# Optimization experiments

Hardware: AMD Instinct MI355X
Metric: run time of the kernel (lower is better)

Reference implementation:

```python
import jax, jax.numpy as jnp
import numpy as np

ALPHA = 1.0
BETA = 2.0
GAMMA = 1.5  # PositionEffectFunction default (config.gamma is NOT passed through)
TEMPERATURE = 1.0


def position_matrix(L: int) -> jnp.ndarray:
    idx = jnp.arange(L, dtype=jnp.float32)
    dist = jnp.abs(idx[:, None] - idx[None, :]) / L  # normalized |i-j|/L
    base = jnp.exp(-BETA * dist)
    return ALPHA * (1.0 + GAMMA * base) / (1.0 + GAMMA)  # [L, L]


def setup_inputs() -> dict:
    key = jax.random.key(0)
    ks = jax.random.split(key, 10)
    B, S, D = 8, 2048, 1024
    std = 0.02
    return {
        "x": jax.random.normal(ks[0], (B, S, D), jnp.float32),
        "pos_emb": jax.random.normal(ks[1], (1, S, D), jnp.float32),
        "Wq": jax.random.normal(ks[2], (D, D), jnp.float32) * std,
        "bq": jax.random.normal(ks[3], (D,), jnp.float32) * std,
        "Wk": jax.random.normal(ks[4], (D, D), jnp.float32) * std,
        "bk": jax.random.normal(ks[5], (D,), jnp.float32) * std,
        "Wv": jax.random.normal(ks[6], (D, D), jnp.float32) * std,
        "bv": jax.random.normal(ks[7], (D,), jnp.float32) * std,
        "Wo": jax.random.normal(ks[8], (D, D), jnp.float32) * std,
        "bo": jax.random.normal(ks[9], (D,), jnp.float32) * std,
    }


def reference(x, pos_emb, Wq, bq, Wk, bk, Wv, bv, Wo, bo):
    B, S, D = x.shape
    x = x + pos_emb[:, :S, :]
    Q = x @ Wq + bq  # [B,S,D]
    K = x @ Wk + bk
    V = x @ Wv + bv
    scores = jnp.einsum("bsd,btd->bst", Q, K) / jnp.sqrt(jnp.float32(D))
    pw = position_matrix(S)  # [S,S], broadcast over batch
    scores = scores * pw[None, :, :] / TEMPERATURE
    attn = jax.nn.softmax(scores, axis=-1)  # [B,S,S]
    out = jnp.einsum("bst,btd->bsd", attn, V)
    out = out @ Wo + bo
    return out, attn
```

## Files before the change

kernel.cpp:

```cpp
#include <hip/hip_runtime.h>
#include <hip/hip_bf16.h>
#include <cstdint>

typedef _Float16 f16x8 __attribute__((ext_vector_type(8)));
typedef _Float16 f16x4 __attribute__((ext_vector_type(4)));
typedef float    f32x4 __attribute__((ext_vector_type(4)));

static constexpr int B = 8, S = 2048, D = 1024;
static constexpr long BSD = (long)B * S * D;
static constexpr long SD  = (long)S * D;
static constexpr long SS  = (long)S * S;
static constexpr long DD  = (long)D * D;

__device__ __forceinline__ void gload16(const void* g, void* l) {
  __builtin_amdgcn_global_load_lds(
      (const __attribute__((address_space(1))) void*)g,
      (__attribute__((address_space(3))) void*)l, 16, 0, 0);
}

#define CFENCE() asm volatile("" ::: "memory")

__global__ __launch_bounds__(256) void prep_x_kernel(
    const float* __restrict__ x, const float* __restrict__ pos,
    _Float16* __restrict__ xh) {
  long i = ((long)blockIdx.x * 256 + threadIdx.x) * 4;
  float4 xv = *(const float4*)(x + i);
  long p = i & (SD - 1);
  float4 pv = *(const float4*)(pos + p);
  f16x4 h;
  h.x = (_Float16)(xv.x + pv.x);
  h.y = (_Float16)(xv.y + pv.y);
  h.z = (_Float16)(xv.z + pv.z);
  h.w = (_Float16)(xv.w + pv.w);
  *(f16x4*)(xh + i) = h;
}

__global__ __launch_bounds__(256) void prep_w_kernel(
    const float* __restrict__ Wq, const float* __restrict__ Wk,
    const float* __restrict__ Wv, const float* __restrict__ Wo,
    _Float16* __restrict__ wqkv, _Float16* __restrict__ woh) {
  __shared__ _Float16 t[64][65];
  const int c0 = blockIdx.x * 64;
  const int r0 = blockIdx.y * 64;
  const int tid = threadIdx.x;
  const int lc = tid & 63;
  const int lr4 = tid >> 6;
  const float* srcs[4] = {Wq, Wk, Wv, Wo};
  #pragma unroll
  for (int m = 0; m < 4; ++m) {
    const float* src = srcs[m];
    _Float16* dst = (m < 3) ? (wqkv + (long)m * DD) : woh;
    #pragma unroll
    for (int ii = 0; ii < 16; ++ii) {
      int row = ii * 4 + lr4;
      t[lc][row] = (_Float16)src[(long)(r0 + row) * D + c0 + lc];
    }
    __syncthreads();
    #pragma unroll
    for (int ii = 0; ii < 16; ++ii) {
      int orow = ii * 4 + lr4;
      dst[(long)(c0 + orow) * D + r0 + lc] = t[orow][lc];
    }
    __syncthreads();
  }
}

__global__ __launch_bounds__(256) void prep_misc_kernel(
    const float* __restrict__ bq, const float* __restrict__ bk,
    const float* __restrict__ bv,
    float* __restrict__ bcat, float* __restrict__ pwtab) {
  int i = blockIdx.x * 256 + threadIdx.x;
  if (i < 3072) {
    float v = (i < 1024) ? bq[i] : (i < 2048) ? bk[i - 1024] : bv[i - 2048];
    bcat[i] = v;
  }
  int d = i - 3072;
  if (d >= 0 && d < 2048) {
    float dist = (float)d * (1.0f / 2048.0f);
    pwtab[d] = (1.0f + 1.5f * expf(-2.0f * dist)) * (1.0f / 2.5f) * (1.0f / 32.0f);
  }
}


enum { EPI_QKV = 0, EPI_SF16 = 1, EPI_PVO = 2, EPI_F32B = 3 };

__device__ __forceinline__ void stage_half(
    char* smem, const _Float16* mb, int off, int k64K, int sthb,
    int dst0, int dst1) {
  gload16(mb + off, smem + sthb + dst0);
  gload16(mb + off + k64K, smem + sthb + dst1);
}

__device__ __forceinline__ void rdA(const char* p, f16x8 (&af)[4][2]) {
#pragma unroll
  for (int mr = 0; mr < 4; ++mr)
#pragma unroll
    for (int kk = 0; kk < 2; ++kk)
      af[mr][kk] = *(const f16x8*)(p + mr * 2048 + kk * 1024);
}

__device__ __forceinline__ void rdB(const char* p, f16x8 (&bf)[2][2]) {
#pragma unroll
  for (int nr = 0; nr < 2; ++nr)
#pragma unroll
    for (int kk = 0; kk < 2; ++kk)
      bf[nr][kk] = *(const f16x8*)(p + nr * 2048 + kk * 1024);
}

__device__ __forceinline__ void mfma16(const f16x8 (&af)[4][2],
                                       const f16x8 (&bf)[2][2],
                                       f32x4 (&a4)[4][2]) {
#pragma unroll
  for (int kk = 0; kk < 2; ++kk)
#pragma unroll
    for (int mr = 0; mr < 4; ++mr)
#pragma unroll
      for (int nr = 0; nr < 2; ++nr)
        a4[mr][nr] = __builtin_amdgcn_mfma_f32_16x16x32_f16(
            af[mr][kk], bf[nr][kk], a4[mr][nr], 0, 0, 0);
}

template<int EPI>
__global__ __launch_bounds__(512, 2) void gemm256_kernel(
    const _Float16* __restrict__ A, const _Float16* __restrict__ Bt,
    const float* __restrict__ bias, const float* __restrict__ pwtab,
    float* __restrict__ outF,
    _Float16* __restrict__ o0, _Float16* __restrict__ o1, _Float16* __restrict__ o2,
    int M, int N, int K, long sA, long sB, long sC)
{
  __shared__ __align__(16) char smem[131072];
  const int tid = threadIdx.x;
  const int z = blockIdx.z;

  int bx = blockIdx.x, by = blockIdx.y;
  if (gridDim.z == 1) {
    const int bid = by * gridDim.x + bx;
    const int idx = bid >> 3;
    by = ((bid & 7) << 3) + (idx & 7);
    bx = idx >> 3;
  }
  const int rb = by * 256;
  const int cb = bx * 256;
  const _Float16* Ag = A + (long)z * sA + (long)rb * K;
  const _Float16* Bg = Bt + (long)z * sB + (long)cb * K;

  const int lane = tid & 63;
  const int wid = tid >> 6;
  const int lrin = lane & 15;
  const int lhi = lane >> 4;
  const int rtail = (lrin * 64 + lhi * 16) ^ (((lane >> 3) & 1) << 5);
  const int aoff = ((wid >> 2) * 4) * 2048 + rtail;
  const int boff = ((wid & 3) * 2) * 2048 + rtail;

  const int rin = lane >> 2;
  const int cinp = (lane & 3) ^ (((lane >> 5) & 1) << 1);
  const int rowc = (wid >> 1) * 16 + rin;
  const int colc = (wid & 1) * 32 + cinp * 8;
  const int stBase = rowc * K + colc;
  const int k64K = 64 * K;
  const int h128K = 128 * K;
  const int dst0 = tid * 16;
  const int dst1 = 8192 + tid * 16;

  const int NT = K >> 6;
  f32x4 acc00[4][2] = {}, acc01[4][2] = {}, acc11[4][2] = {}, acc10[4][2] = {};

  stage_half(smem, Ag, stBase,              k64K, 0,             dst0, dst1);
  stage_half(smem, Bg, stBase,              k64K, 32768,         dst0, dst1);
  stage_half(smem, Ag, stBase + h128K,      k64K, 16384,         dst0, dst1);
  stage_half(smem, Bg, stBase + h128K,      k64K, 49152,         dst0, dst1);
  stage_half(smem, Ag, stBase + 64,         k64K, 65536,         dst0, dst1);
  stage_half(smem, Bg, stBase + h128K + 64, k64K, 65536 + 49152, dst0, dst1);
  asm volatile("s_waitcnt vmcnt(4)" ::: "memory");
  __builtin_amdgcn_s_barrier();
  CFENCE();

  for (int t = 0; t < NT; ++t) {
    const int curbase = (t & 1) << 16;
    const int nxtbase = curbase ^ 65536;
    const bool s1ok = (t + 1) < NT;
    const bool s2ok = (t + 2) < NT;
    const int st1 = stBase + (t + 1) * 64;
    const int st2 = stBase + (t + 2) * 64;
    f16x8 af[4][2], bfA[2][2], bfB[2][2];

    rdA((const char*)smem + curbase + aoff, af);
    rdB((const char*)smem + curbase + 32768 + boff, bfA);
    if (s1ok) stage_half(smem, Ag, st1 + h128K, k64K, nxtbase + 16384, dst0, dst1);
    CFENCE();
    __builtin_amdgcn_s_barrier();
    CFENCE();
    __builtin_amdgcn_s_setprio(1);
    mfma16(af, bfA, acc00);
    __builtin_amdgcn_s_setprio(0);
    CFENCE();
    __builtin_amdgcn_s_barrier();
    CFENCE();

    rdB((const char*)smem + curbase + 49152 + boff, bfB);
    if (s1ok) stage_half(smem, Bg, st1, k64K, nxtbase + 32768, dst0, dst1);
    CFENCE();
    __builtin_amdgcn_s_barrier();
    CFENCE();
    __builtin_amdgcn_s_setprio(1);
    mfma16(af, bfB, acc01);
    __builtin_amdgcn_s_setprio(0);
    CFENCE();
    __builtin_amdgcn_s_barrier();
    CFENCE();

    rdA((const char*)smem + curbase + 16384 + aoff, af);
    if (s2ok) stage_half(smem, Ag, st2, k64K, curbase + 0, dst0, dst1);
    CFENCE();
    __builtin_amdgcn_s_barrier();
    CFENCE();
    __builtin_amdgcn_s_setprio(1);
    mfma16(af, bfB, acc11);
    __builtin_amdgcn_s_setprio(0);
    CFENCE();
    __builtin_amdgcn_s_barrier();
    CFENCE();

    rdB((const char*)smem + curbase + 32768 + boff, bfA);
    if (s2ok) stage_half(smem, Bg, st2 + h128K, k64K, curbase + 49152, dst0, dst1);
    CFENCE();
    __builtin_amdgcn_s_barrier();
    CFENCE();
    __builtin_amdgcn_s_setprio(1);
    mfma16(af, bfA, acc10);
    __builtin_amdgcn_s_setprio(0);
    if (s2ok) {
      asm volatile("s_waitcnt vmcnt(4)" ::: "memory");
    } else {
      asm volatile("s_waitcnt vmcnt(0)" ::: "memory");
    }
    __builtin_amdgcn_s_barrier();
    CFENCE();
  }

  const int wrow = (wid >> 2) * 64;
  const int wcol = (wid & 3) * 32;
  auto epi = [&](const f32x4 (&a4)[4][2], int qm, int qn) {
#pragma unroll
    for (int nr = 0; nr < 2; ++nr) {
      const int col = cb + qn * 128 + wcol + nr * 16 + lrin;
      float bv = 0.0f;
      if (EPI == EPI_QKV || EPI == EPI_F32B) bv = bias[col];
#pragma unroll
      for (int mr = 0; mr < 4; ++mr) {
        const int rowb = rb + qm * 128 + wrow + mr * 16 + lhi * 4;
        const f32x4 v4 = a4[mr][nr];
#pragma unroll
        for (int r = 0; r < 4; ++r) {
          const int row = rowb + r;
          const float v = v4[r];
          if (EPI == EPI_QKV) {
            const int matid = cb >> 10;
            _Float16* dst = (matid == 0) ? o0 : (matid == 1) ? o1 : o2;
            const int cl = col & 1023;
            const float vb = v + bv;
            if (matid < 2) {
              dst[(long)row * 1024 + cl] = (_Float16)vb;
            } else {
              const int bb = row >> 11;
              const int trow = row & (S - 1);
              dst[(long)bb * SD + (long)cl * S + trow] = (_Float16)vb;
            }
          } else if (EPI == EPI_SF16) {
            int dd = row - col; if (dd < 0) dd = -dd;
            o0[(long)z * sC + (long)row * N + col] = (_Float16)(v * pwtab[dd]);
          } else if (EPI == EPI_PVO) {
            o0[(long)z * sC + (long)row * N + col] = (_Float16)v;
          } else {
            outF[(long)row * N + col] = v + bv;
          }
        }
      }
    }
  };
  epi(acc00, 0, 0);
  epi(acc01, 0, 1);
  epi(acc11, 1, 1);
  epi(acc10, 1, 0);
}

__global__ __launch_bounds__(256) void softmax_kernel(
    const _Float16* __restrict__ sbf, float* __restrict__ attn,
    _Float16* __restrict__ abf) {
  const long base = (long)blockIdx.x * S + threadIdx.x * 8;
  const int tid = threadIdx.x;
  const f16x8 sv = *(const f16x8*)(sbf + base);
  float v[8];
  #pragma unroll
  for (int t = 0; t < 8; ++t) v[t] = (float)sv[t];
  float m = fmaxf(fmaxf(fmaxf(v[0], v[1]), fmaxf(v[2], v[3])),
                  fmaxf(fmaxf(v[4], v[5]), fmaxf(v[6], v[7])));
  #pragma unroll
  for (int sh = 1; sh < 64; sh <<= 1) m = fmaxf(m, __shfl_xor(m, sh));
  __shared__ float red[8];
  const int w = tid >> 6;
  if ((tid & 63) == 0) red[w] = m;
  __syncthreads();
  m = fmaxf(fmaxf(red[0], red[1]), fmaxf(red[2], red[3]));
  float e[8];
  #pragma unroll
  for (int t = 0; t < 8; ++t) e[t] = expf(v[t] - m);
  float s8 = ((e[0] + e[1]) + (e[2] + e[3])) + ((e[4] + e[5]) + (e[6] + e[7]));
  #pragma unroll
  for (int sh = 1; sh < 64; sh <<= 1) s8 += __shfl_xor(s8, sh);
  if ((tid & 63) == 0) red[4 + w] = s8;
  __syncthreads();
  const float inv = 1.0f / ((red[4] + red[5]) + (red[6] + red[7]));
  float4 o0 = make_float4(e[0] * inv, e[1] * inv, e[2] * inv, e[3] * inv);
  float4 o1 = make_float4(e[4] * inv, e[5] * inv, e[6] * inv, e[7] * inv);
  *(float4*)(attn + base) = o0;
  *(float4*)(attn + base + 4) = o1;
  f16x8 hb;
  hb[0] = (_Float16)o0.x; hb[1] = (_Float16)o0.y;
  hb[2] = (_Float16)o0.z; hb[3] = (_Float16)o0.w;
  hb[4] = (_Float16)o1.x; hb[5] = (_Float16)o1.y;
  hb[6] = (_Float16)o1.z; hb[7] = (_Float16)o1.w;
  *(f16x8*)(abf + base) = hb;
}

extern "C" void kernel_launch(void* const* d_in, const int* in_sizes, int n_in,
                              void* d_out, int out_size, void* d_ws, size_t ws_size,
                              hipStream_t stream) {
  const float* x   = (const float*)d_in[0];
  const float* pos = (const float*)d_in[1];
  const float* Wq  = (const float*)d_in[2];
  const float* bq  = (const float*)d_in[3];
  const float* Wk  = (const float*)d_in[4];
  const float* bk  = (const float*)d_in[5];
  const float* Wv  = (const float*)d_in[6];
  const float* bv  = (const float*)d_in[7];
  const float* Wo  = (const float*)d_in[8];
  const float* bo  = (const float*)d_in[9];

  float* outp  = (float*)d_out;
  float* attnp = outp + BSD;

  _Float16* wqkv = (_Float16*)d_ws;
  _Float16* woh  = wqkv + 3 * DD;
  float*    bcat = (float*)(woh + DD);
  float*    pwtab = bcat + 3072;
  _Float16* qh  = (_Float16*)(pwtab + 2048);
  _Float16* kh  = qh + BSD;
  _Float16* vt  = kh + BSD;
  _Float16* sbf = vt + BSD;
  _Float16* abf = sbf + (long)B * SS;
  _Float16* hbf = qh;

  _Float16* xph = (_Float16*)attnp;

  dim3 blk(256);
  prep_w_kernel<<<dim3(16, 16), blk, 0, stream>>>(Wq, Wk, Wv, Wo, wqkv, woh);
  prep_misc_kernel<<<dim3(20), blk, 0, stream>>>(bq, bk, bv, bcat, pwtab);
  prep_x_kernel<<<dim3((int)(BSD / 1024)), blk, 0, stream>>>(x, pos, xph);

  dim3 blk5(512);
  gemm256_kernel<EPI_QKV><<<dim3(12, 64, 1), blk5, 0, stream>>>(
      xph, wqkv, bcat, nullptr, nullptr, qh, kh, vt, B * S, 3 * D, D, 0, 0, 0);

  gemm256_kernel<EPI_SF16><<<dim3(8, 8, B), blk5, 0, stream>>>(
      qh, kh, nullptr, pwtab, nullptr, sbf, nullptr, nullptr, S, S, D, SD, SD, SS);

  softmax_kernel<<<dim3(B * S), blk, 0, stream>>>(sbf, attnp, abf);

  gemm256_kernel<EPI_PVO><<<dim3(4, 8, B), blk5, 0, stream>>>(
      abf, vt, nullptr, nullptr, nullptr, hbf, nullptr, nullptr, S, D, S, SS, SD, SD);

  gemm256_kernel<EPI_F32B><<<dim3(4, 64, 1), blk5, 0, stream>>>(
      hbf, woh, bo, nullptr, outp, nullptr, nullptr, nullptr, B * S, D, D, 0, 0, 0);
}
```

Measured before the change: 436.3 us.

## Drop redundant GEMM loop barriers and stage V-transpose epilogue through LDS

```diff
diff --git a/kernel.cpp b/kernel.cpp
--- a/kernel.cpp
+++ b/kernel.cpp
@@ -193,9 +193,6 @@
     __builtin_amdgcn_s_setprio(1);
     mfma16(af, bfA, acc00);
     __builtin_amdgcn_s_setprio(0);
-    CFENCE();
-    __builtin_amdgcn_s_barrier();
-    CFENCE();
 
     rdB((const char*)smem + curbase + 49152 + boff, bfB);
     if (s1ok) stage_half(smem, Bg, st1, k64K, nxtbase + 32768, dst0, dst1);
@@ -205,9 +202,6 @@
     __builtin_amdgcn_s_setprio(1);
     mfma16(af, bfB, acc01);
     __builtin_amdgcn_s_setprio(0);
-    CFENCE();
-    __builtin_amdgcn_s_barrier();
-    CFENCE();
 
     rdA((const char*)smem + curbase + 16384 + aoff, af);
     if (s2ok) stage_half(smem, Ag, st2, k64K, curbase + 0, dst0, dst1);
@@ -217,71 +211,98 @@
     __builtin_amdgcn_s_setprio(1);
     mfma16(af, bfB, acc11);
     __builtin_amdgcn_s_setprio(0);
-    CFENCE();
-    __builtin_amdgcn_s_barrier();
-    CFENCE();
 
     rdB((const char*)smem + curbase + 32768 + boff, bfA);
     if (s2ok) stage_half(smem, Bg, st2 + h128K, k64K, curbase + 49152, dst0, dst1);
-    CFENCE();
-    __builtin_amdgcn_s_barrier();
-    CFENCE();
-    __builtin_amdgcn_s_setprio(1);
-    mfma16(af, bfA, acc10);
-    __builtin_amdgcn_s_setprio(0);
     if (s2ok) {
       asm volatile("s_waitcnt vmcnt(4)" ::: "memory");
     } else {
       asm volatile("s_waitcnt vmcnt(0)" ::: "memory");
     }
+    CFENCE();
     __builtin_amdgcn_s_barrier();
     CFENCE();
+    __builtin_amdgcn_s_setprio(1);
+    mfma16(af, bfA, acc10);
+    __builtin_amdgcn_s_setprio(0);
   }
 
   const int wrow = (wid >> 2) * 64;
   const int wcol = (wid & 3) * 32;
-  auto epi = [&](const f32x4 (&a4)[4][2], int qm, int qn) {
-#pragma unroll
-    for (int nr = 0; nr < 2; ++nr) {
-      const int col = cb + qn * 128 + wcol + nr * 16 + lrin;
-      float bv = 0.0f;
-      if (EPI == EPI_QKV || EPI == EPI_F32B) bv = bias[col];
-#pragma unroll
-      for (int mr = 0; mr < 4; ++mr) {
-        const int rowb = rb + qm * 128 + wrow + mr * 16 + lhi * 4;
-        const f32x4 v4 = a4[mr][nr];
-#pragma unroll
-        for (int r = 0; r < 4; ++r) {
-          const int row = rowb + r;
-          const float v = v4[r];
-          if (EPI == EPI_QKV) {
-            const int matid = cb >> 10;
-            _Float16* dst = (matid == 0) ? o0 : (matid == 1) ? o1 : o2;
-            const int cl = col & 1023;
-            const float vb = v + bv;
-            if (matid < 2) {
-              dst[(long)row * 1024 + cl] = (_Float16)vb;
+  const int matid = (EPI == EPI_QKV) ? (cb >> 10) : 0;
+
+  if (EPI == EPI_QKV && matid == 2) {
+    __syncthreads();
+    auto vfrag = [&](const f32x4 (&a4)[4][2], int qm, int qn) {
+#pragma unroll
+      for (int nr = 0; nr < 2; ++nr) {
+        const int dl = qn * 128 + wcol + nr * 16 + lrin;
+        const float bv = bias[cb + dl];
+        const int xr = (dl & 7) << 4;
+#pragma unroll
+        for (int mr = 0; mr < 4; ++mr) {
+          const int tl = qm * 128 + wrow + mr * 16 + lhi * 4;
+          const f32x4 v4 = a4[mr][nr];
+          f16x4 p;
+          p[0] = (_Float16)(v4[0] + bv);
+          p[1] = (_Float16)(v4[1] + bv);
+          p[2] = (_Float16)(v4[2] + bv);
+          p[3] = (_Float16)(v4[3] + bv);
+          *(f16x4*)(smem + dl * 512 + ((tl * 2) ^ xr)) = p;
+        }
+      }
+    };
+    vfrag(acc00, 0, 0);
+    vfrag(acc01, 0, 1);
+    vfrag(acc11, 1, 1);
+    vfrag(acc10, 1, 0);
+    __syncthreads();
+    const int t0 = rb & (S - 1);
+    const int bbk = rb >> 11;
+    const int lr5 = tid & 31;
+    const int dr0 = tid >> 5;
+#pragma unroll
+    for (int pass = 0; pass < 16; ++pass) {
+      const int dl = pass * 16 + dr0;
+      const f16x8 vv = *(const f16x8*)(smem + dl * 512 + ((lr5 * 16) ^ ((dl & 7) << 4)));
+      *(f16x8*)(o2 + (long)bbk * SD + (long)(cb - 2048 + dl) * S + t0 + lr5 * 8) = vv;
+    }
+  } else {
+    auto epi = [&](const f32x4 (&a4)[4][2], int qm, int qn) {
+#pragma unroll
+      for (int nr = 0; nr < 2; ++nr) {
+        const int col = cb + qn * 128 + wcol + nr * 16 + lrin;
+        float bv = 0.0f;
+        if (EPI == EPI_QKV || EPI == EPI_F32B) bv = bias[col];
+#pragma unroll
+        for (int mr = 0; mr < 4; ++mr) {
+          const int rowb = rb + qm * 128 + wrow + mr * 16 + lhi * 4;
+          const f32x4 v4 = a4[mr][nr];
+#pragma unroll
+          for (int r = 0; r < 4; ++r) {
+            const int row = rowb + r;
+            const float v = v4[r];
+            if (EPI == EPI_QKV) {
+              _Float16* dst = (matid == 0) ? o0 : o1;
+              const int cl = col & 1023;
+              dst[(long)row * 1024 + cl] = (_Float16)(v + bv);
+            } else if (EPI == EPI_SF16) {
+              int dd = row - col; if (dd < 0) dd = -dd;
+              o0[(long)z * sC + (long)row * N + col] = (_Float16)(v * pwtab[dd]);
+            } else if (EPI == EPI_PVO) {
+              o0[(long)z * sC + (long)row * N + col] = (_Float16)v;
             } else {
-              const int bb = row >> 11;
-              const int trow = row & (S - 1);
-              dst[(long)bb * SD + (long)cl * S + trow] = (_Float16)vb;
+              outF[(long)row * N + col] = v + bv;
             }
-          } else if (EPI == EPI_SF16) {
-            int dd = row - col; if (dd < 0) dd = -dd;
-            o0[(long)z * sC + (long)row * N + col] = (_Float16)(v * pwtab[dd]);
-          } else if (EPI == EPI_PVO) {
-            o0[(long)z * sC + (long)row * N + col] = (_Float16)v;
-          } else {
-            outF[(long)row * N + col] = v + bv;
           }
         }
       }
-    }
-  };
-  epi(acc00, 0, 0);
-  epi(acc01, 0, 1);
-  epi(acc11, 1, 1);
-  epi(acc10, 1, 0);
+    };
+    epi(acc00, 0, 0);
+    epi(acc01, 0, 1);
+    epi(acc11, 1, 1);
+    epi(acc10, 1, 0);
+  }
 }
 
 __global__ __launch_bounds__(256) void softmax_kernel(
```

Result: faster. 378.7 us (-13.2%).
